# Kernel tuning notes

Hardware: AMD Instinct MI355X
Metric: run time of the kernel (lower is better)

Reference implementation:

```python
import jax, jax.numpy as jnp
import numpy as np

NEG_INF = -1e30  # stands in for torch's -inf diagonal mask; exp() underflows to 0 identically


def conv1x1(x, w, b):
    # x: [B,C,H,W], w: [O,C], b: [O]
    return jnp.einsum('oc,bchw->bohw', w, x) + b[None, :, None, None]


def s_module(x, qw, qb, kw, kb, vw, vb, gamma):
    # CCNet criss-cross attention with -inf diagonal masking on the H branch.
    B, C, H, W = x.shape
    q = conv1x1(x, qw, qb)  # [B,C8,H,W]
    k = conv1x1(x, kw, kb)  # [B,C8,H,W]
    v = conv1x1(x, vw, vb)  # [B,C,H,W]
    # energy_H[b,h,w,g] = <q[b,:,h,w], k[b,:,g,w]>  (attend along column)
    e_h = jnp.einsum('bchw,bcgw->bhwg', q, k)
    diag_mask = jnp.where(jnp.eye(H, dtype=bool), NEG_INF, 0.0).astype(x.dtype)
    e_h = e_h + diag_mask[None, :, None, :]  # mask h == g
    # energy_W[b,h,w,v] = <q[b,:,h,w], k[b,:,h,v]>  (attend along row)
    e_w = jnp.einsum('bchw,bchv->bhwv', q, k)
    att = jax.nn.softmax(jnp.concatenate([e_h, e_w], axis=-1), axis=-1)  # [B,H,W,H+W]
    a_h, a_w = att[..., :H], att[..., H:]
    out_h = jnp.einsum('bcgw,bhwg->bchw', v, a_h)
    out_w = jnp.einsum('bchv,bhwv->bchw', v, a_w)
    return gamma * (out_h + out_w) + x


def cam_module(x, fb, gamma):
    # channel attention: energy [B,C,C], max-sub trick, softmax, bmm back
    B, C, H, W = x.shape
    f = fb.reshape(B, C, H * W)
    energy = jnp.einsum('bcn,bdn->bcd', f, f)
    energy_new = jnp.max(energy, axis=-1, keepdims=True) - energy
    att = jax.nn.softmax(energy_new, axis=-1)
    out = jnp.einsum('bcd,bdn->bcn', att, f).reshape(B, C, H, W)
    return x + gamma * out


def _forward(x, fb, w_conv, b_conv, bn_g, bn_b,
             xq_w, xq_b, xk_w, xk_b, xv_w, xv_b, x_gamma,
             fq_w, fq_b, fk_w, fk_b, fv_w, fv_b, f_gamma,
             pam_gamma, pam_gamma2, cam_gamma):
    # MaxPool2d(kernel=2, stride=2)
    fbd = jax.lax.reduce_window(fb, -jnp.inf, jax.lax.max,
                                (1, 1, 2, 2), (1, 1, 2, 2), 'VALID')
    # convblock: 1x1 conv + BatchNorm (training-mode batch stats) + ReLU
    y = conv1x1(fbd, w_conv, b_conv)
    mu = jnp.mean(y, axis=(0, 2, 3), keepdims=True)
    var = jnp.var(y, axis=(0, 2, 3), keepdims=True)
    y = (y - mu) * jax.lax.rsqrt(var + 1e-5)
    y = y * bn_g[None, :, None, None] + bn_b[None, :, None, None]
    y = jax.nn.relu(y)
    # FeedbackSpatialAttention (PAM)
    x_att = pam_gamma * s_module(x, xq_w, xq_b, xk_w, xk_b, xv_w, xv_b, x_gamma)
    fb_att = s_module(y, fq_w, fq_b, fk_w, fk_b, fv_w, fv_b, f_gamma)
    pam_out = x + x_att + pam_gamma2 * fb_att
    # CAM on (x, processed fb)
    cam_out = cam_module(x, y, cam_gamma)
    return pam_out + cam_out


def setup_inputs() -> dict:
    key = jax.random.key(0)
    ks = jax.random.split(key, 24)
    B, C, H, W = 4, 64, 128, 128
    C8 = C // 8
    d = {
        'x': jax.random.normal(ks[0], (B, C, H, W), jnp.float32),
        'fb': jax.random.normal(ks[1], (B, C, 2 * H, 2 * W), jnp.float32),
        'w_conv': jax.random.normal(ks[2], (C, C), jnp.float32) * 0.05,
        'b_conv': jax.random.normal(ks[3], (C,), jnp.float32) * 0.02,
        'bn_g': jax.random.uniform(ks[4], (C,), jnp.float32, 0.5, 1.5),
        'bn_b': jax.random.normal(ks[5], (C,), jnp.float32) * 0.02,
        'xq_w': jax.random.normal(ks[6], (C8, C), jnp.float32) * 0.05,
        'xq_b': jax.random.normal(ks[7], (C8,), jnp.float32) * 0.02,
        'xk_w': jax.random.normal(ks[8], (C8, C), jnp.float32) * 0.05,
        'xk_b': jax.random.normal(ks[9], (C8,), jnp.float32) * 0.02,
        'xv_w': jax.random.normal(ks[10], (C, C), jnp.float32) * 0.05,
        'xv_b': jax.random.normal(ks[11], (C,), jnp.float32) * 0.02,
        'x_gamma': jax.random.normal(ks[12], (1,), jnp.float32) * 0.1,
        'fq_w': jax.random.normal(ks[13], (C8, C), jnp.float32) * 0.05,
        'fq_b': jax.random.normal(ks[14], (C8,), jnp.float32) * 0.02,
        'fk_w': jax.random.normal(ks[15], (C8, C), jnp.float32) * 0.05,
        'fk_b': jax.random.normal(ks[16], (C8,), jnp.float32) * 0.02,
        'fv_w': jax.random.normal(ks[17], (C, C), jnp.float32) * 0.05,
        'fv_b': jax.random.normal(ks[18], (C,), jnp.float32) * 0.02,
        'f_gamma': jax.random.normal(ks[19], (1,), jnp.float32) * 0.1,
        'pam_gamma': jax.random.normal(ks[20], (1,), jnp.float32) * 0.1,
        'pam_gamma2': jax.random.normal(ks[21], (1,), jnp.float32) * 0.1,
        'cam_gamma': jax.random.normal(ks[22], (1,), jnp.float32) * 0.1,
    }
    return d


def reference(x, fb, w_conv, b_conv, bn_g, bn_b,
              xq_w, xq_b, xk_w, xk_b, xv_w, xv_b, x_gamma,
              fq_w, fq_b, fk_w, fk_b, fv_w, fv_b, f_gamma,
              pam_gamma, pam_gamma2, cam_gamma):
    return _forward(x, fb, w_conv, b_conv, bn_g, bn_b,
                    xq_w, xq_b, xk_w, xk_b, xv_w, xv_b, x_gamma,
                    fq_w, fq_b, fk_w, fk_b, fv_w, fv_b, f_gamma,
                    pam_gamma, pam_gamma2, cam_gamma)
```

## Files before the change

### kernel.cpp

```cpp
#include <hip/hip_runtime.h>
#include <hip/hip_bf16.h>

#define NP 16384
#define NB 4

typedef __hip_bfloat16 bf16;
typedef unsigned short u16;
typedef unsigned short us8 __attribute__((ext_vector_type(8)));
typedef unsigned short us4 __attribute__((ext_vector_type(4)));
typedef short ss8 __attribute__((ext_vector_type(8)));
typedef float f32x4 __attribute__((ext_vector_type(4)));
__device__ __forceinline__ float bf2f(const bf16 v) { return __bfloat162float(v); }
__device__ __forceinline__ bf16 f2bf(float v) { return __float2bfloat16(v); }
__device__ __forceinline__ float bfu(u16 h) {
  return __uint_as_float(((unsigned)h) << 16);
}
__device__ __forceinline__ u16 fbu(float v) {
  bf16 b = f2bf(v);
  return *(u16*)&b;
}


__global__ __launch_bounds__(256, 4) void k_pool_conv(
    const float* __restrict__ fb, const float* __restrict__ wconv,
    const float* __restrict__ bconv, bf16* __restrict__ Y) {
  __shared__ __align__(16) u16 Xs[64 * 64];
  __shared__ __align__(16) u16 wHi[64 * 64], wLo[64 * 64];
  __shared__ float bS[64];
  int tid = threadIdx.x;
  int b = blockIdx.x >> 8, tile = blockIdx.x & 255;
  int n0 = tile * 64;
  int h = n0 >> 7, w0 = n0 & 127;
  for (int i = tid; i < 4096; i += 256) {
    int oc = i >> 6, c = i & 63;
    float wv = wconv[oc * 64 + c];
    u16 hb = fbu(wv);
    u16 lb = fbu(wv - bfu(hb));
    int idx = i ^ ((oc & 7) << 3);
    wHi[idx] = hb;
    wLo[idx] = lb;
  }
  if (tid < 64) bS[tid] = bconv[tid];
  for (int i2 = tid; i2 < 2048; i2 += 256) {
    int c = i2 >> 5, pp = i2 & 31;
    const float* r0 =
        fb + ((size_t)((b * 64 + c) * 256 + 2 * h)) * 256 + 2 * w0 + 4 * pp;
    float4 v0 = *(const float4*)r0;
    float4 v1 = *(const float4*)(r0 + 256);
    int px = 2 * pp;
    float a0 = fmaxf(fmaxf(v0.x, v0.y), fmaxf(v1.x, v1.y));
    float a1 = fmaxf(fmaxf(v0.z, v0.w), fmaxf(v1.z, v1.w));
    Xs[(px * 64 + c) ^ ((((px & 7) ^ ((px >> 3) & 7))) << 3)] = fbu(a0);
    px++;
    Xs[(px * 64 + c) ^ ((((px & 7) ^ ((px >> 3) & 7))) << 3)] = fbu(a1);
  }
  __syncthreads();
  int lane = tid & 63, wv = tid >> 6;
  int il = lane & 15, gq = lane >> 4;
  int pxb = wv * 16;
  ss8 afr[2];
#pragma unroll
  for (int ks = 0; ks < 2; ++ks) {
    int px = pxb + il;
    int idx =
        (px * 64 + ks * 32 + gq * 8) ^ ((((px & 7) ^ ((px >> 3) & 7))) << 3);
    afr[ks] = *(const ss8*)&Xs[idx];
  }
#pragma unroll
  for (int oct = 0; oct < 4; ++oct) {
    int oc = oct * 16 + il;
    ss8 wh[2], wl[2];
#pragma unroll
    for (int ks = 0; ks < 2; ++ks) {
      int idx = (oc * 64 + ks * 32 + gq * 8) ^ ((oc & 7) << 3);
      wh[ks] = *(const ss8*)&wHi[idx];
      wl[ks] = *(const ss8*)&wLo[idx];
    }
    float bv = bS[oc];
    f32x4 acc = {bv, bv, bv, bv};
#pragma unroll
    for (int ks = 0; ks < 2; ++ks) {
      acc = __builtin_amdgcn_mfma_f32_16x16x32_bf16(afr[ks], wh[ks], acc, 0, 0, 0);
      acc = __builtin_amdgcn_mfma_f32_16x16x32_bf16(afr[ks], wl[ks], acc, 0, 0, 0);
    }
    int px0 = pxb + gq * 4;
    us4 ov;
#pragma unroll
    for (int r = 0; r < 4; ++r) ov[r] = fbu(acc[r]);
    *(us4*)(Y + (size_t)(b * 64 + oc) * NP + n0 + px0) = ov;
  }
}

__global__ __launch_bounds__(256) void k_stats_p1(const bf16* __restrict__ Y,
                                                  float* __restrict__ PS) {
  int blk = blockIdx.x, tid = threadIdx.x;
  int o = blk >> 3, slab = blk & 7;
  int b = slab >> 1, half = slab & 1;
  const us8* vp =
      (const us8*)(Y + ((size_t)(b * 64 + o)) * NP + half * 8192);
  float s = 0.f, ss = 0.f;
#pragma unroll
  for (int it = 0; it < 4; ++it) {
    us8 v = vp[tid + 256 * it];
#pragma unroll
    for (int e = 0; e < 8; ++e) {
      float f = bfu(v[e]);
      s += f;
      ss = fmaf(f, f, ss);
    }
  }
  for (int off = 32; off > 0; off >>= 1) {
    s += __shfl_down(s, off, 64);
    ss += __shfl_down(ss, off, 64);
  }
  __shared__ float sh[8];
  int wv = tid >> 6, ln = tid & 63;
  if (ln == 0) { sh[wv] = s; sh[4 + wv] = ss; }
  __syncthreads();
  if (tid == 0) {
    PS[blk] = sh[0] + sh[1] + sh[2] + sh[3];
    PS[512 + blk] = sh[4] + sh[5] + sh[6] + sh[7];
  }
}

__global__ __launch_bounds__(64) void k_stats_p2(
    const float* __restrict__ PS, const float* __restrict__ bng,
    const float* __restrict__ bnb, float* __restrict__ SCALE,
    float* __restrict__ SHIFT, const float* xg, const float* fg,
    const float* pg, const float* pg2, const float* cg,
    float* __restrict__ HDR) {
  int o = threadIdx.x;
  float s = 0.f, ss = 0.f;
#pragma unroll
  for (int k = 0; k < 8; ++k) {
    s += PS[o * 8 + k];
    ss += PS[512 + o * 8 + k];
  }
  const float inv = 1.0f / (NB * NP);
  float mu = s * inv;
  float var = ss * inv - mu * mu;
  float r = rsqrtf(var + 1e-5f);
  float sc = r * bng[o];
  SCALE[o] = sc;
  SHIFT[o] = bnb[o] - mu * sc;
  if (o == 0) {
    float vpg = pg[0];
    HDR[1] = vpg * xg[0];
    HDR[2] = pg2[0] * fg[0];
    HDR[3] = 2.0f + vpg;
    HDR[4] = pg2[0];
    HDR[5] = cg[0];
  }
}

__global__ __launch_bounds__(256, 4) void k_conv_mfma(
    const float* __restrict__ xin, const bf16* __restrict__ Yin,
    const float* __restrict__ SCALE, const float* __restrict__ SHIFT,
    const float* __restrict__ qw0, const float* __restrict__ qb0,
    const float* __restrict__ kw0, const float* __restrict__ kb0,
    const float* __restrict__ vw0, const float* __restrict__ vb0,
    const float* __restrict__ qw1, const float* __restrict__ qb1,
    const float* __restrict__ kw1, const float* __restrict__ kb1,
    const float* __restrict__ vw1, const float* __restrict__ vb1,
    bf16* __restrict__ QK, bf16* __restrict__ V) {
  __shared__ __align__(16) u16 Xs[128 * 64];
  __shared__ __align__(16) u16 wHi[80 * 64], wLo[80 * 64];
  __shared__ float bS[80];
  int tid = threadIdx.x;
  int m = blockIdx.x >> 9;
  int b = (blockIdx.x >> 7) & 3;
  int tile = blockIdx.x & 127;
  int n0 = tile * 128;
  const float* qw = m ? qw1 : qw0;
  const float* qb = m ? qb1 : qb0;
  const float* kw = m ? kw1 : kw0;
  const float* kb = m ? kb1 : kb0;
  const float* vw = m ? vw1 : vw0;
  const float* vb = m ? vb1 : vb0;
  for (int i = tid; i < 5120; i += 256) {
    int oc = i >> 6, c = i & 63;
    float w;
    if (oc < 8) w = qw[oc * 64 + c];
    else if (oc < 16) w = kw[(oc - 8) * 64 + c];
    else w = vw[(oc - 16) * 64 + c];
    u16 hb = fbu(w);
    u16 lb = fbu(w - bfu(hb));
    int idx = (oc * 64 + c) ^ ((oc & 7) << 3);
    wHi[idx] = hb;
    wLo[idx] = lb;
  }
  if (tid < 80)
    bS[tid] = (tid < 8) ? qb[tid] : (tid < 16) ? kb[tid - 8] : vb[tid - 16];
  if (m) {
    for (int i2 = tid; i2 < 1024; i2 += 256) {
      int c = i2 >> 4, vj = i2 & 15;
      us8 v = *(const us8*)(Yin + (size_t)(b * 64 + c) * NP + n0 + vj * 8);
      float sc = SCALE[c], sh = SHIFT[c];
#pragma unroll
      for (int e = 0; e < 8; ++e) {
        int px = vj * 8 + e;
        float f = fmaxf(fmaf(bfu(v[e]), sc, sh), 0.f);
        Xs[(px * 64 + c) ^ ((((px & 7) ^ ((px >> 3) & 7))) << 3)] = fbu(f);
      }
    }
  } else {
    for (int i2 = tid; i2 < 2048; i2 += 256) {
      int c = i2 >> 5, vj = i2 & 31;
      float4 v = *(const float4*)(xin + (size_t)(b * 64 + c) * NP + n0 + vj * 4);
      float vv[4] = {v.x, v.y, v.z, v.w};
#pragma unroll
      for (int r = 0; r < 4; ++r) {
        int px = vj * 4 + r;
        Xs[(px * 64 + c) ^ ((((px & 7) ^ ((px >> 3) & 7))) << 3)] = fbu(vv[r]);
      }
    }
  }
  __syncthreads();
  int lane = tid & 63, wv = tid >> 6;
  int il = lane & 15, gq = lane >> 4;
  int pxb = wv * 32;
  ss8 afr[2][2];
#pragma unroll
  for (int sub = 0; sub < 2; ++sub)
#pragma unroll
    for (int ks = 0; ks < 2; ++ks) {
      int px = pxb + sub * 16 + il;
      int idx =
          (px * 64 + ks * 32 + gq * 8) ^ ((((px & 7) ^ ((px >> 3) & 7))) << 3);
      afr[sub][ks] = *(const ss8*)&Xs[idx];
    }
#pragma unroll
  for (int oct = 0; oct < 5; ++oct) {
    int oc = oct * 16 + il;
    ss8 wh[2], wl[2];
#pragma unroll
    for (int ks = 0; ks < 2; ++ks) {
      int idx = (oc * 64 + ks * 32 + gq * 8) ^ ((oc & 7) << 3);
      wh[ks] = *(const ss8*)&wHi[idx];
      wl[ks] = *(const ss8*)&wLo[idx];
    }
    float bv = bS[oc];
    bf16* dst;
    size_t basep;
    if (oc < 8) { dst = QK; basep = (size_t)(((m * 2 + 0) * 4 + b) * 8 + oc) * NP; }
    else if (oc < 16) { dst = QK; basep = (size_t)(((m * 2 + 1) * 4 + b) * 8 + (oc - 8)) * NP; }
    else { dst = V; basep = (size_t)((m * 4 + b) * 64 + (oc - 16)) * NP; }
#pragma unroll
    for (int sub = 0; sub < 2; ++sub) {
      f32x4 acc = {bv, bv, bv, bv};
#pragma unroll
      for (int ks = 0; ks < 2; ++ks) {
        acc = __builtin_amdgcn_mfma_f32_16x16x32_bf16(afr[sub][ks], wh[ks], acc, 0, 0, 0);
        acc = __builtin_amdgcn_mfma_f32_16x16x32_bf16(afr[sub][ks], wl[ks], acc, 0, 0, 0);
      }
      int px0 = pxb + sub * 16 + gq * 4;
      us4 ov;
#pragma unroll
      for (int r = 0; r < 4; ++r) ov[r] = fbu(acc[r]);
      *(us4*)(dst + basep + n0 + px0) = ov;
    }
  }
}

__global__ __launch_bounds__(256) void k_transpose2(
    const u16* __restrict__ inA, u16* __restrict__ outA,
    const u16* __restrict__ inB, u16* __restrict__ outB, int nA) {
  int tileId = blockIdx.x & 15;
  int plane = blockIdx.x >> 4;
  const u16* ip;
  u16* op;
  if (plane < nA) {
    ip = inA + (size_t)plane * NP;
    op = outA + (size_t)plane * NP;
  } else {
    ip = inB + (size_t)(plane - nA) * NP;
    op = outB + (size_t)(plane - nA) * NP;
  }
  int th = tileId >> 2, tw = tileId & 3;
  __shared__ u16 t[32][33];
  int lx = threadIdx.x & 31, ly = threadIdx.x >> 5;
  for (int i = 0; i < 32; i += 8)
    t[ly + i][lx] = ip[(size_t)(th * 32 + ly + i) * 128 + tw * 32 + lx];
  __syncthreads();
  for (int i = 0; i < 32; i += 8)
    op[(size_t)(tw * 32 + ly + i) * 128 + th * 32 + lx] = t[lx][ly + i];
}

__global__ __launch_bounds__(256, 4) void k_av(
    const bf16* __restrict__ QK, const bf16* __restrict__ QKT,
    const bf16* __restrict__ V, const bf16* __restrict__ VT,
    float* __restrict__ MWp, float* __restrict__ LWp,
    float* __restrict__ MHp, float* __restrict__ LHp,
    float* __restrict__ OW, bf16* __restrict__ OHT) {
  int blk = blockIdx.x;
  int m = blk & 1, mode = (blk >> 1) & 1;
  int bid = blk >> 2;
  int b = bid >> 7, h = bid & 127;
  const bf16* qkbase = mode ? QKT : QK;
  const bf16* Qp = qkbase + (size_t)(((m * 2 + 0) * 4 + b) * 8) * NP;
  const bf16* Kp = qkbase + (size_t)(((m * 2 + 1) * 4 + b) * 8) * NP;
  const bf16* Vp = (mode ? VT : V) + (size_t)((m * 4 + b) * 64) * NP;
  __shared__ __align__(16) u16 qT[128 * 8];
  __shared__ __align__(16) u16 kT[128 * 8];
  __shared__ __align__(16) u16 Vs[64 * 136];
  int tid = threadIdx.x;
  {
    int c = (tid >> 4) & 7, vj = tid & 15;
    const bf16* src = (tid < 128) ? Qp : Kp;
    u16* dst = (tid < 128) ? qT : kT;
    const us8* sp = (const us8*)(src + (size_t)c * NP + (size_t)h * 128);
    us8 sv = sp[vj];
#pragma unroll
    for (int e = 0; e < 8; ++e) {
      int j = vj * 8 + e;
      int p = ((j & 7) << 4) | (j >> 3);
      dst[p * 8 + c] = sv[e];
    }
  }
  for (int i2 = tid; i2 < 1024; i2 += 256) {
    int c = i2 >> 4, vj = i2 & 15;
    const us8* vp = (const us8*)(Vp + (size_t)c * NP + (size_t)h * 128);
    us8 vv = vp[vj];
    *(us8*)&Vs[c * 136 + vj * 8] = vv;
  }
  __syncthreads();
  int lane = tid & 63, wv = tid >> 6;
  int il = lane & 15, gq = lane >> 4;
  size_t sb = (size_t)(m * 4 + b) * NP;
  float* owBase = OW + (size_t)((m * 4 + b) * 64) * NP + (size_t)h * 128;
  bf16* ohBase = OHT + (size_t)((m * 4 + b) * 64) * NP + (size_t)h * 128;
#pragma unroll
  for (int sub = 0; sub < 2; ++sub) {
    int ib = wv * 32 + sub * 16;
    int i = ib + il;
    int pi = ((i & 7) << 4) | (i >> 3);
    us8 qv = *(const us8*)&qT[pi * 8];
    float qr[8];
#pragma unroll
    for (int c = 0; c < 8; ++c) qr[c] = bfu(qv[c]);
    float scr[4][8];
    float mrow = -3.0e38f;
#pragma unroll
    for (int ks = 0; ks < 4; ++ks) {
#pragma unroll
      for (int e = 0; e < 8; ++e) {
        int j = ks * 32 + gq * 8 + e;
        int pj = ((j & 7) << 4) | (j >> 3);
        us8 kv = *(const us8*)&kT[pj * 8];
        float s = 0.f;
#pragma unroll
        for (int c = 0; c < 8; ++c) s = fmaf(qr[c], bfu(kv[c]), s);
        if (mode && j == i) s = -1.0e30f;
        scr[ks][e] = s;
        mrow = fmaxf(mrow, s);
      }
    }
    mrow = fmaxf(mrow, __shfl_xor(mrow, 16, 64));
    mrow = fmaxf(mrow, __shfl_xor(mrow, 32, 64));
    float l = 0.f;
    ss8 afr[4];
#pragma unroll
    for (int ks = 0; ks < 4; ++ks) {
      ss8 af;
#pragma unroll
      for (int e = 0; e < 8; ++e) {
        float ev = __expf(scr[ks][e] - mrow);
        l += ev;
        af[e] = (short)fbu(ev);
      }
      afr[ks] = af;
    }
    l += __shfl_xor(l, 16, 64);
    l += __shfl_xor(l, 32, 64);
    if (gq == 0) {
      if (mode == 0) {
        MWp[sb + (size_t)h * 128 + i] = mrow;
        LWp[sb + (size_t)h * 128 + i] = l;
      } else {
        MHp[sb + (size_t)i * 128 + h] = mrow;
        LHp[sb + (size_t)i * 128 + h] = l;
      }
    }
#pragma unroll
    for (int ct = 0; ct < 4; ++ct) {
      f32x4 acc = {0.f, 0.f, 0.f, 0.f};
#pragma unroll
      for (int ks = 0; ks < 4; ++ks) {
        ss8 bv = *(const ss8*)&Vs[(ct * 16 + il) * 136 + ks * 32 + gq * 8];
        acc = __builtin_amdgcn_mfma_f32_16x16x32_bf16(afr[ks], bv, acc, 0, 0, 0);
      }
      int cch = ct * 16 + il;
      int i0 = ib + gq * 4;
      if (mode == 0) {
#pragma unroll
        for (int r = 0; r < 4; ++r)
          owBase[(size_t)cch * NP + (size_t)(i0 + r)] = acc[r];
      } else {
#pragma unroll
        for (int r = 0; r < 4; ++r)
          ohBase[(size_t)cch * NP + (size_t)(i0 + r)] = f2bf(acc[r]);
      }
    }
  }
}

__global__ __launch_bounds__(256) void k_merge2(
    const bf16* __restrict__ OHT, const float* __restrict__ OW,
    const float* __restrict__ MWp, const float* __restrict__ LWp,
    const float* __restrict__ MHp, const float* __restrict__ LHp,
    const float* __restrict__ HDR, float* __restrict__ ACC) {
  int tileId = blockIdx.x & 15;
  int plane = blockIdx.x >> 4;
  int b = plane >> 6;
  int th = tileId >> 2, tw = tileId & 3;
  __shared__ float t0[32][33], t1[32][33];
  int lx = threadIdx.x & 31, ly = threadIdx.x >> 5;
  const bf16* ip0 = OHT + (size_t)plane * NP;
  const bf16* ip1 = OHT + (size_t)(256 + plane) * NP;
  for (int i = 0; i < 32; i += 8) {
    size_t idx = (size_t)(th * 32 + ly + i) * 128 + tw * 32 + lx;
    t0[ly + i][lx] = bf2f(ip0[idx]);
    t1[ly + i][lx] = bf2f(ip1[idx]);
  }
  __syncthreads();
  float sc0 = HDR[1], sc1 = HDR[2];
  float* op = ACC + (size_t)plane * NP;
  const float* ow0 = OW + (size_t)plane * NP;
  const float* ow1 = OW + (size_t)(256 + plane) * NP;
  size_t s0 = (size_t)b * NP, s1 = (size_t)(4 + b) * NP;
  for (int i = 0; i < 32; i += 8) {
    int hh = tw * 32 + ly + i, ww = th * 32 + lx;
    size_t idx = (size_t)hh * 128 + ww;
    float mw0 = MWp[s0 + idx], mh0 = MHp[s0 + idx];
    float M0 = fmaxf(mw0, mh0);
    float ea0 = __expf(mw0 - M0), eb0 = __expf(mh0 - M0);
    float inv0 = 1.0f / (LWp[s0 + idx] * ea0 + LHp[s0 + idx] * eb0);
    float v0 = (ea0 * ow0[idx] + eb0 * t0[lx][ly + i]) * inv0;
    float mw1 = MWp[s1 + idx], mh1 = MHp[s1 + idx];
    float M1 = fmaxf(mw1, mh1);
    float ea1 = __expf(mw1 - M1), eb1 = __expf(mh1 - M1);
    float inv1 = 1.0f / (LWp[s1 + idx] * ea1 + LHp[s1 + idx] * eb1);
    float v1 = (ea1 * ow1[idx] + eb1 * t1[lx][ly + i]) * inv1;
    op[idx] = sc0 * v0 + sc1 * v1;
  }
}

__global__ __launch_bounds__(256) void k_gram(const bf16* __restrict__ Y,
                                              const float* __restrict__ SCALE,
                                              const float* __restrict__ SHIFT,
                                              float* __restrict__ GP) {
  int b = blockIdx.x >> 7, ch = (blockIdx.x >> 2) & 31, t = blockIdx.x & 3;
  int tid = threadIdx.x;
  __shared__ float fs[64 * 129];
  int cg = tid >> 4, dg = tid & 15;
  float acc[4][4];
#pragma unroll
  for (int i = 0; i < 4; ++i)
#pragma unroll
    for (int jx = 0; jx < 4; ++jx) acc[i][jx] = 0.f;
  const bf16* yb = Y + (size_t)b * 64 * NP + ch * 512;
  for (int idx = tid; idx < 8192; idx += 256) {
    int c = idx >> 7, j = idx & 127;
    float v = fmaf(bf2f(yb[(size_t)c * NP + t * 128 + j]), SCALE[c], SHIFT[c]);
    fs[c * 129 + j] = fmaxf(v, 0.f);
  }
  __syncthreads();
  for (int j = 0; j < 128; ++j) {
    float a[4], d[4];
#pragma unroll
    for (int i = 0; i < 4; ++i) a[i] = fs[(cg * 4 + i) * 129 + j];
#pragma unroll
    for (int i = 0; i < 4; ++i) d[i] = fs[(dg * 4 + i) * 129 + j];
#pragma unroll
    for (int i = 0; i < 4; ++i)
#pragma unroll
      for (int jx = 0; jx < 4; ++jx) acc[i][jx] = fmaf(a[i], d[jx], acc[i][jx]);
  }
  float* gp = GP + ((size_t)(b * 128) + ch * 4 + t) * 4096;
#pragma unroll
  for (int i = 0; i < 4; ++i)
#pragma unroll
    for (int jx = 0; jx < 4; ++jx)
      gp[(cg * 4 + i) * 64 + dg * 4 + jx] = acc[i][jx];
}

__global__ __launch_bounds__(256) void k_gram_reduce(const float* __restrict__ GP,
                                                     float* __restrict__ CATT) {
  int b = blockIdx.x >> 4, rg = blockIdx.x & 15;
  int tid = threadIdx.x;
  __shared__ float Es[256];
  int e = rg * 256 + tid;
  float s = 0.f;
  for (int k = 0; k < 128; ++k) s += GP[((size_t)b * 128 + k) * 4096 + e];
  Es[tid] = s;
  __syncthreads();
  int wv = tid >> 6, ln = tid & 63;
  float v = Es[wv * 64 + ln];
  float mn = v;
  for (int off = 32; off; off >>= 1) mn = fminf(mn, __shfl_xor(mn, off, 64));
  float ev = __expf(mn - v);
  float ssum = ev;
  for (int off = 32; off; off >>= 1) ssum += __shfl_xor(ssum, off, 64);
  CATT[((size_t)b * 64 + rg * 4 + wv) * 64 + ln] = ev / ssum;
}

__global__ __launch_bounds__(256) void k_final(
    const float* __restrict__ x, const bf16* __restrict__ Y,
    const float* __restrict__ SCALE, const float* __restrict__ SHIFT,
    const float* __restrict__ CATT, const float* __restrict__ HDR,
    float* __restrict__ OUT) {
  __shared__ float attS[64 * 65], Ys[64 * 65];
  int tid = threadIdx.x;
  int b = blockIdx.x >> 8, tile = blockIdx.x & 255;
  int n0 = tile * 64;
  for (int i = tid; i < 4096; i += 256)
    attS[(i >> 6) * 65 + (i & 63)] = CATT[(size_t)b * 4096 + i];
  for (int i = tid; i < 4096; i += 256) {
    int d = i >> 6, px = i & 63;
    float v = fmaf(bf2f(Y[(size_t)(b * 64 + d) * NP + n0 + px]), SCALE[d], SHIFT[d]);
    Ys[d * 65 + px] = fmaxf(v, 0.f);
  }
  __syncthreads();
  int cg = tid >> 4, pgx = tid & 15;
  int c0 = cg * 4, p0 = pgx * 4;
  float acc[4][4];
#pragma unroll
  for (int i = 0; i < 4; ++i)
#pragma unroll
    for (int j = 0; j < 4; ++j) acc[i][j] = 0.f;
  for (int d = 0; d < 64; ++d) {
    float a[4], yv[4];
#pragma unroll
    for (int i = 0; i < 4; ++i) a[i] = attS[(c0 + i) * 65 + d];
#pragma unroll
    for (int j = 0; j < 4; ++j) yv[j] = Ys[d * 65 + p0 + j];
#pragma unroll
    for (int i = 0; i < 4; ++i)
#pragma unroll
      for (int j = 0; j < 4; ++j) acc[i][j] = fmaf(a[i], yv[j], acc[i][j]);
  }
  float c2pg = HDR[3], fpg2 = HDR[4], fcg = HDR[5];
#pragma unroll
  for (int i = 0; i < 4; ++i) {
    size_t base = (size_t)(b * 64 + c0 + i) * NP + n0 + p0;
#pragma unroll
    for (int j = 0; j < 4; ++j) {
      float yv = Ys[(c0 + i) * 65 + p0 + j];
      OUT[base + j] =
          c2pg * x[base + j] + fpg2 * yv + OUT[base + j] + fcg * acc[i][j];
    }
  }
}

extern "C" void kernel_launch(void* const* d_in, const int* in_sizes, int n_in,
                              void* d_out, int out_size, void* d_ws, size_t ws_size,
                              hipStream_t stream) {
  const float* x = (const float*)d_in[0];
  const float* fbp = (const float*)d_in[1];

  char* base = (char*)d_ws;
  float* HDR = (float*)base;
  float* SCALE = HDR + 16;
  float* SHIFT = SCALE + 64;
  char* p = base + 4096;
  bf16* Y = (bf16*)p;    p += 8388608;
  bf16* QK = (bf16*)p;   p += 4194304;
  bf16* QKT = (bf16*)p;  p += 4194304;
  bf16* V = (bf16*)p;    p += 16777216;
  bf16* VT = (bf16*)p;   p += 16777216;
  float* MWp = (float*)p; p += 524288;
  float* LWp = (float*)p; p += 524288;
  float* MHp = (float*)p; p += 524288;
  float* LHp = (float*)p; p += 524288;
  bf16* OHT = (bf16*)p;  p += 16777216;
  float* OW = (float*)p; p += 33554432;
  float* GP = (float*)p; p += 8388608;
  float* CATT = (float*)p; p += 1048576;
  float* ACC = (float*)d_out;
  float* PS = (float*)QK;

  k_pool_conv<<<1024, 256, 0, stream>>>(fbp, (const float*)d_in[2],
                                        (const float*)d_in[3], Y);
  k_stats_p1<<<512, 256, 0, stream>>>(Y, PS);
  k_stats_p2<<<1, 64, 0, stream>>>(PS, (const float*)d_in[4],
                                   (const float*)d_in[5], SCALE, SHIFT,
                                   (const float*)d_in[12], (const float*)d_in[19],
                                   (const float*)d_in[20], (const float*)d_in[21],
                                   (const float*)d_in[22], HDR);

  k_conv_mfma<<<1024, 256, 0, stream>>>(
      x, Y, SCALE, SHIFT,
      (const float*)d_in[6], (const float*)d_in[7], (const float*)d_in[8],
      (const float*)d_in[9], (const float*)d_in[10], (const float*)d_in[11],
      (const float*)d_in[13], (const float*)d_in[14], (const float*)d_in[15],
      (const float*)d_in[16], (const float*)d_in[17], (const float*)d_in[18],
      QK, V);
  k_transpose2<<<10240, 256, 0, stream>>>((const u16*)QK, (u16*)QKT,
                                          (const u16*)V, (u16*)VT, 128);
  k_av<<<2048, 256, 0, stream>>>(QK, QKT, V, VT, MWp, LWp, MHp, LHp, OW, OHT);
  k_merge2<<<4096, 256, 0, stream>>>(OHT, OW, MWp, LWp, MHp, LHp, HDR, ACC);

  k_gram<<<512, 256, 0, stream>>>(Y, SCALE, SHIFT, GP);
  k_gram_reduce<<<64, 256, 0, stream>>>(GP, CATT);
  k_final<<<1024, 256, 0, stream>>>(x, Y, SCALE, SHIFT, CATT, HDR,
                                    (float*)d_out);
}
```

Measured before the change: 277.4 us.

## Fuse BN stats into pool-conv, merge gram into conv, store OW as bf16

The BatchNorm partial sums now come straight from the MFMA accumulators inside the pool+conv kernel, so the separate pass that re-reads Y for statistics is gone. The second stats kernel reduces 1024 per-block partials. The gram kernel is merged into the QKV conv launch as extra blocks, and the gram reduction is merged into the merge kernel, which cuts the launch count. The W-branch output is stored in bf16 instead of fp32, halving that round-trip's traffic at some cost in precision.

Result: slower. 384.0 us (+38.4%).

```diff
diff --git a/kernel.cpp b/kernel.cpp
--- a/kernel.cpp
+++ b/kernel.cpp
@@ -23,17 +23,19 @@
 
 __global__ __launch_bounds__(256, 4) void k_pool_conv(
     const float* __restrict__ fb, const float* __restrict__ wconv,
-    const float* __restrict__ bconv, bf16* __restrict__ Y) {
+    const float* __restrict__ bconv, bf16* __restrict__ Y,
+    float* __restrict__ PS) {
   __shared__ __align__(16) u16 Xs[64 * 64];
   __shared__ __align__(16) u16 wHi[64 * 64], wLo[64 * 64];
   __shared__ float bS[64];
+  __shared__ float redS[256], redSS[256];
   int tid = threadIdx.x;
   int b = blockIdx.x >> 8, tile = blockIdx.x & 255;
   int n0 = tile * 64;
   int h = n0 >> 7, w0 = n0 & 127;
   for (int i = tid; i < 4096; i += 256) {
-    int oc = i >> 6, c = i & 63;
-    float wv = wconv[oc * 64 + c];
+    int oc = i >> 6;
+    float wv = wconv[i];
     u16 hb = fbu(wv);
     u16 lb = fbu(wv - bfu(hb));
     int idx = i ^ ((oc & 7) << 3);
@@ -55,9 +57,9 @@
     Xs[(px * 64 + c) ^ ((((px & 7) ^ ((px >> 3) & 7))) << 3)] = fbu(a1);
   }
   __syncthreads();
-  int lane = tid & 63, wv = tid >> 6;
+  int lane = tid & 63, wvid = tid >> 6;
   int il = lane & 15, gq = lane >> 4;
-  int pxb = wv * 16;
+  int pxb = wvid * 16;
   ss8 afr[2];
 #pragma unroll
   for (int ks = 0; ks < 2; ++ks) {
@@ -88,72 +90,61 @@
 #pragma unroll
     for (int r = 0; r < 4; ++r) ov[r] = fbu(acc[r]);
     *(us4*)(Y + (size_t)(b * 64 + oc) * NP + n0 + px0) = ov;
-  }
-}
-
-__global__ __launch_bounds__(256) void k_stats_p1(const bf16* __restrict__ Y,
-                                                  float* __restrict__ PS) {
-  int blk = blockIdx.x, tid = threadIdx.x;
-  int o = blk >> 3, slab = blk & 7;
-  int b = slab >> 1, half = slab & 1;
-  const us8* vp =
-      (const us8*)(Y + ((size_t)(b * 64 + o)) * NP + half * 8192);
-  float s = 0.f, ss = 0.f;
-#pragma unroll
-  for (int it = 0; it < 4; ++it) {
-    us8 v = vp[tid + 256 * it];
-#pragma unroll
-    for (int e = 0; e < 8; ++e) {
-      float f = bfu(v[e]);
-      s += f;
-      ss = fmaf(f, f, ss);
-    }
-  }
-  for (int off = 32; off > 0; off >>= 1) {
-    s += __shfl_down(s, off, 64);
-    ss += __shfl_down(ss, off, 64);
-  }
-  __shared__ float sh[8];
-  int wv = tid >> 6, ln = tid & 63;
-  if (ln == 0) { sh[wv] = s; sh[4 + wv] = ss; }
-  __syncthreads();
-  if (tid == 0) {
-    PS[blk] = sh[0] + sh[1] + sh[2] + sh[3];
-    PS[512 + blk] = sh[4] + sh[5] + sh[6] + sh[7];
-  }
-}
-
-__global__ __launch_bounds__(64) void k_stats_p2(
+    float s_oc = (acc[0] + acc[1]) + (acc[2] + acc[3]);
+    float ss_oc = fmaf(acc[0], acc[0],
+                  fmaf(acc[1], acc[1], fmaf(acc[2], acc[2], acc[3] * acc[3])));
+    s_oc += __shfl_xor(s_oc, 16, 64);
+    s_oc += __shfl_xor(s_oc, 32, 64);
+    ss_oc += __shfl_xor(ss_oc, 16, 64);
+    ss_oc += __shfl_xor(ss_oc, 32, 64);
+    if (gq == 0) { redS[wvid * 64 + oc] = s_oc; redSS[wvid * 64 + oc] = ss_oc; }
+  }
+  __syncthreads();
+  if (tid < 128) {
+    int st = tid >> 6, oc = tid & 63;
+    const float* rr = st ? redSS : redS;
+    PS[(size_t)blockIdx.x * 128 + tid] =
+        (rr[oc] + rr[64 + oc]) + (rr[128 + oc] + rr[192 + oc]);
+  }
+}
+
+__global__ __launch_bounds__(256) void k_stats_p2(
     const float* __restrict__ PS, const float* __restrict__ bng,
     const float* __restrict__ bnb, float* __restrict__ SCALE,
     float* __restrict__ SHIFT, const float* xg, const float* fg,
     const float* pg, const float* pg2, const float* cg,
     float* __restrict__ HDR) {
-  int o = threadIdx.x;
-  float s = 0.f, ss = 0.f;
-#pragma unroll
-  for (int k = 0; k < 8; ++k) {
-    s += PS[o * 8 + k];
-    ss += PS[512 + o * 8 + k];
-  }
-  const float inv = 1.0f / (NB * NP);
-  float mu = s * inv;
-  float var = ss * inv - mu * mu;
-  float r = rsqrtf(var + 1e-5f);
-  float sc = r * bng[o];
-  SCALE[o] = sc;
-  SHIFT[o] = bnb[o] - mu * sc;
-  if (o == 0) {
-    float vpg = pg[0];
-    HDR[1] = vpg * xg[0];
-    HDR[2] = pg2[0] * fg[0];
-    HDR[3] = 2.0f + vpg;
-    HDR[4] = pg2[0];
-    HDR[5] = cg[0];
-  }
-}
-
-__global__ __launch_bounds__(256, 4) void k_conv_mfma(
+  int t = threadIdx.x;
+  __shared__ float sh[256];
+  int s = t & 127, half = t >> 7;
+  float a = 0.f;
+  for (int blk = half * 512; blk < half * 512 + 512; ++blk)
+    a += PS[(size_t)blk * 128 + s];
+  sh[t] = a;
+  __syncthreads();
+  if (t < 128) sh[t] = sh[t] + sh[128 + t];
+  __syncthreads();
+  if (t < 64) {
+    float ssum = sh[t], sqs = sh[64 + t];
+    const float inv = 1.0f / (NB * NP);
+    float mu = ssum * inv;
+    float var = sqs * inv - mu * mu;
+    float r = rsqrtf(var + 1e-5f);
+    float sc = r * bng[t];
+    SCALE[t] = sc;
+    SHIFT[t] = bnb[t] - mu * sc;
+    if (t == 0) {
+      float vpg = pg[0];
+      HDR[1] = vpg * xg[0];
+      HDR[2] = pg2[0] * fg[0];
+      HDR[3] = 2.0f + vpg;
+      HDR[4] = pg2[0];
+      HDR[5] = cg[0];
+    }
+  }
+}
+
+__global__ __launch_bounds__(256, 4) void k_conv_gram(
     const float* __restrict__ xin, const bf16* __restrict__ Yin,
     const float* __restrict__ SCALE, const float* __restrict__ SHIFT,
     const float* __restrict__ qw0, const float* __restrict__ qb0,
@@ -162,103 +153,141 @@
     const float* __restrict__ qw1, const float* __restrict__ qb1,
     const float* __restrict__ kw1, const float* __restrict__ kb1,
     const float* __restrict__ vw1, const float* __restrict__ vb1,
-    bf16* __restrict__ QK, bf16* __restrict__ V) {
-  __shared__ __align__(16) u16 Xs[128 * 64];
-  __shared__ __align__(16) u16 wHi[80 * 64], wLo[80 * 64];
-  __shared__ float bS[80];
+    bf16* __restrict__ QK, bf16* __restrict__ V, float* __restrict__ GP) {
+  __shared__ __align__(16) char SMEM[37248];
   int tid = threadIdx.x;
-  int m = blockIdx.x >> 9;
-  int b = (blockIdx.x >> 7) & 3;
-  int tile = blockIdx.x & 127;
-  int n0 = tile * 128;
-  const float* qw = m ? qw1 : qw0;
-  const float* qb = m ? qb1 : qb0;
-  const float* kw = m ? kw1 : kw0;
-  const float* kb = m ? kb1 : kb0;
-  const float* vw = m ? vw1 : vw0;
-  const float* vb = m ? vb1 : vb0;
-  for (int i = tid; i < 5120; i += 256) {
-    int oc = i >> 6, c = i & 63;
-    float w;
-    if (oc < 8) w = qw[oc * 64 + c];
-    else if (oc < 16) w = kw[(oc - 8) * 64 + c];
-    else w = vw[(oc - 16) * 64 + c];
-    u16 hb = fbu(w);
-    u16 lb = fbu(w - bfu(hb));
-    int idx = (oc * 64 + c) ^ ((oc & 7) << 3);
-    wHi[idx] = hb;
-    wLo[idx] = lb;
-  }
-  if (tid < 80)
-    bS[tid] = (tid < 8) ? qb[tid] : (tid < 16) ? kb[tid - 8] : vb[tid - 16];
-  if (m) {
-    for (int i2 = tid; i2 < 1024; i2 += 256) {
-      int c = i2 >> 4, vj = i2 & 15;
-      us8 v = *(const us8*)(Yin + (size_t)(b * 64 + c) * NP + n0 + vj * 8);
-      float sc = SCALE[c], sh = SHIFT[c];
-#pragma unroll
-      for (int e = 0; e < 8; ++e) {
-        int px = vj * 8 + e;
-        float f = fmaxf(fmaf(bfu(v[e]), sc, sh), 0.f);
-        Xs[(px * 64 + c) ^ ((((px & 7) ^ ((px >> 3) & 7))) << 3)] = fbu(f);
+  if (blockIdx.x < 1024) {
+    u16* Xs = (u16*)SMEM;
+    u16* wHi = (u16*)(SMEM + 16384);
+    u16* wLo = (u16*)(SMEM + 26624);
+    float* bS = (float*)(SMEM + 36864);
+    int m = blockIdx.x >> 9;
+    int b = (blockIdx.x >> 7) & 3;
+    int tile = blockIdx.x & 127;
+    int n0 = tile * 128;
+    const float* qw = m ? qw1 : qw0;
+    const float* qb = m ? qb1 : qb0;
+    const float* kw = m ? kw1 : kw0;
+    const float* kb = m ? kb1 : kb0;
+    const float* vw = m ? vw1 : vw0;
+    const float* vb = m ? vb1 : vb0;
+    for (int i = tid; i < 5120; i += 256) {
+      int oc = i >> 6, c = i & 63;
+      float w;
+      if (oc < 8) w = qw[oc * 64 + c];
+      else if (oc < 16) w = kw[(oc - 8) * 64 + c];
+      else w = vw[(oc - 16) * 64 + c];
+      u16 hb = fbu(w);
+      u16 lb = fbu(w - bfu(hb));
+      int idx = (oc * 64 + c) ^ ((oc & 7) << 3);
+      wHi[idx] = hb;
+      wLo[idx] = lb;
+    }
+    if (tid < 80)
+      bS[tid] = (tid < 8) ? qb[tid] : (tid < 16) ? kb[tid - 8] : vb[tid - 16];
+    if (m) {
+      for (int i2 = tid; i2 < 1024; i2 += 256) {
+        int c = i2 >> 4, vj = i2 & 15;
+        us8 v = *(const us8*)(Yin + (size_t)(b * 64 + c) * NP + n0 + vj * 8);
+        float sc = SCALE[c], sh = SHIFT[c];
+#pragma unroll
+        for (int e = 0; e < 8; ++e) {
+          int px = vj * 8 + e;
+          float f = fmaxf(fmaf(bfu(v[e]), sc, sh), 0.f);
+          Xs[(px * 64 + c) ^ ((((px & 7) ^ ((px >> 3) & 7))) << 3)] = fbu(f);
+        }
+      }
+    } else {
+      for (int i2 = tid; i2 < 2048; i2 += 256) {
+        int c = i2 >> 5, vj = i2 & 31;
+        float4 v = *(const float4*)(xin + (size_t)(b * 64 + c) * NP + n0 + vj * 4);
+        float vv[4] = {v.x, v.y, v.z, v.w};
+#pragma unroll
+        for (int r = 0; r < 4; ++r) {
+          int px = vj * 4 + r;
+          Xs[(px * 64 + c) ^ ((((px & 7) ^ ((px >> 3) & 7))) << 3)] = fbu(vv[r]);
+        }
+      }
+    }
+    __syncthreads();
+    int lane = tid & 63, wvid = tid >> 6;
+    int il = lane & 15, gq = lane >> 4;
+    int pxb = wvid * 32;
+    ss8 afr[2][2];
+#pragma unroll
+    for (int sub = 0; sub < 2; ++sub)
+#pragma unroll
+      for (int ks = 0; ks < 2; ++ks) {
+        int px = pxb + sub * 16 + il;
+        int idx =
+            (px * 64 + ks * 32 + gq * 8) ^ ((((px & 7) ^ ((px >> 3) & 7))) << 3);
+        afr[sub][ks] = *(const ss8*)&Xs[idx];
+      }
+#pragma unroll
+    for (int oct = 0; oct < 5; ++oct) {
+      int oc = oct * 16 + il;
+      ss8 wh[2], wl[2];
+#pragma unroll
+      for (int ks = 0; ks < 2; ++ks) {
+        int idx = (oc * 64 + ks * 32 + gq * 8) ^ ((oc & 7) << 3);
+        wh[ks] = *(const ss8*)&wHi[idx];
+        wl[ks] = *(const ss8*)&wLo[idx];
+      }
+      float bv = bS[oc];
+      bf16* dst;
+      size_t basep;
+      if (oc < 8) { dst = QK; basep = (size_t)(((m * 2 + 0) * 4 + b) * 8 + oc) * NP; }
+      else if (oc < 16) { dst = QK; basep = (size_t)(((m * 2 + 1) * 4 + b) * 8 + (oc - 8)) * NP; }
+      else { dst = V; basep = (size_t)((m * 4 + b) * 64 + (oc - 16)) * NP; }
+#pragma unroll
+      for (int sub = 0; sub < 2; ++sub) {
+        f32x4 acc = {bv, bv, bv, bv};
+#pragma unroll
+        for (int ks = 0; ks < 2; ++ks) {
+          acc = __builtin_amdgcn_mfma_f32_16x16x32_bf16(afr[sub][ks], wh[ks], acc, 0, 0, 0);
+          acc = __builtin_amdgcn_mfma_f32_16x16x32_bf16(afr[sub][ks], wl[ks], acc, 0, 0, 0);
+        }
+        int px0 = pxb + sub * 16 + gq * 4;
+        us4 ov;
+#pragma unroll
+        for (int r = 0; r < 4; ++r) ov[r] = fbu(acc[r]);
+        *(us4*)(dst + basep + n0 + px0) = ov;
       }
     }
   } else {
-    for (int i2 = tid; i2 < 2048; i2 += 256) {
-      int c = i2 >> 5, vj = i2 & 31;
-      float4 v = *(const float4*)(xin + (size_t)(b * 64 + c) * NP + n0 + vj * 4);
-      float vv[4] = {v.x, v.y, v.z, v.w};
-#pragma unroll
-      for (int r = 0; r < 4; ++r) {
-        int px = vj * 4 + r;
-        Xs[(px * 64 + c) ^ ((((px & 7) ^ ((px >> 3) & 7))) << 3)] = fbu(vv[r]);
-      }
-    }
-  }
-  __syncthreads();
-  int lane = tid & 63, wv = tid >> 6;
-  int il = lane & 15, gq = lane >> 4;
-  int pxb = wv * 32;
-  ss8 afr[2][2];
-#pragma unroll
-  for (int sub = 0; sub < 2; ++sub)
-#pragma unroll
-    for (int ks = 0; ks < 2; ++ks) {
-      int px = pxb + sub * 16 + il;
-      int idx =
-          (px * 64 + ks * 32 + gq * 8) ^ ((((px & 7) ^ ((px >> 3) & 7))) << 3);
-      afr[sub][ks] = *(const ss8*)&Xs[idx];
-    }
-#pragma unroll
-  for (int oct = 0; oct < 5; ++oct) {
-    int oc = oct * 16 + il;
-    ss8 wh[2], wl[2];
-#pragma unroll
-    for (int ks = 0; ks < 2; ++ks) {
-      int idx = (oc * 64 + ks * 32 + gq * 8) ^ ((oc & 7) << 3);
-      wh[ks] = *(const ss8*)&wHi[idx];
-      wl[ks] = *(const ss8*)&wLo[idx];
-    }
-    float bv = bS[oc];
-    bf16* dst;
-    size_t basep;
-    if (oc < 8) { dst = QK; basep = (size_t)(((m * 2 + 0) * 4 + b) * 8 + oc) * NP; }
-    else if (oc < 16) { dst = QK; basep = (size_t)(((m * 2 + 1) * 4 + b) * 8 + (oc - 8)) * NP; }
-    else { dst = V; basep = (size_t)((m * 4 + b) * 64 + (oc - 16)) * NP; }
-#pragma unroll
-    for (int sub = 0; sub < 2; ++sub) {
-      f32x4 acc = {bv, bv, bv, bv};
-#pragma unroll
-      for (int ks = 0; ks < 2; ++ks) {
-        acc = __builtin_amdgcn_mfma_f32_16x16x32_bf16(afr[sub][ks], wh[ks], acc, 0, 0, 0);
-        acc = __builtin_amdgcn_mfma_f32_16x16x32_bf16(afr[sub][ks], wl[ks], acc, 0, 0, 0);
-      }
-      int px0 = pxb + sub * 16 + gq * 4;
-      us4 ov;
-#pragma unroll
-      for (int r = 0; r < 4; ++r) ov[r] = fbu(acc[r]);
-      *(us4*)(dst + basep + n0 + px0) = ov;
-    }
+    float* fs = (float*)SMEM;
+    int bid = blockIdx.x - 1024;
+    int b = bid >> 7, ch = (bid >> 2) & 31, t = bid & 3;
+    int cg = tid >> 4, dg = tid & 15;
+    float acc[4][4];
+#pragma unroll
+    for (int i = 0; i < 4; ++i)
+#pragma unroll
+      for (int jx = 0; jx < 4; ++jx) acc[i][jx] = 0.f;
+    const bf16* yb = Yin + (size_t)b * 64 * NP + ch * 512;
+    for (int idx = tid; idx < 8192; idx += 256) {
+      int c = idx >> 7, j = idx & 127;
+      float v = fmaf(bf2f(yb[(size_t)c * NP + t * 128 + j]), SCALE[c], SHIFT[c]);
+      fs[c * 129 + j] = fmaxf(v, 0.f);
+    }
+    __syncthreads();
+    for (int j = 0; j < 128; ++j) {
+      float a[4], d[4];
+#pragma unroll
+      for (int i = 0; i < 4; ++i) a[i] = fs[(cg * 4 + i) * 129 + j];
+#pragma unroll
+      for (int i = 0; i < 4; ++i) d[i] = fs[(dg * 4 + i) * 129 + j];
+#pragma unroll
+      for (int i = 0; i < 4; ++i)
+#pragma unroll
+        for (int jx = 0; jx < 4; ++jx) acc[i][jx] = fmaf(a[i], d[jx], acc[i][jx]);
+    }
+    float* gp = GP + ((size_t)(b * 128) + ch * 4 + t) * 4096;
+#pragma unroll
+    for (int i = 0; i < 4; ++i)
+#pragma unroll
+      for (int jx = 0; jx < 4; ++jx)
+        gp[(cg * 4 + i) * 64 + dg * 4 + jx] = acc[i][jx];
   }
 }
 
@@ -291,7 +320,7 @@
     const bf16* __restrict__ V, const bf16* __restrict__ VT,
     float* __restrict__ MWp, float* __restrict__ LWp,
     float* __restrict__ MHp, float* __restrict__ LHp,
-    float* __restrict__ OW, bf16* __restrict__ OHT) {
+    bf16* __restrict__ OWb, bf16* __restrict__ OHT) {
   int blk = blockIdx.x;
   int m = blk & 1, mode = (blk >> 1) & 1;
   int bid = blk >> 2;
@@ -324,14 +353,14 @@
     *(us8*)&Vs[c * 136 + vj * 8] = vv;
   }
   __syncthreads();
-  int lane = tid & 63, wv = tid >> 6;
+  int lane = tid & 63, wvid = tid >> 6;
   int il = lane & 15, gq = lane >> 4;
   size_t sb = (size_t)(m * 4 + b) * NP;
-  float* owBase = OW + (size_t)((m * 4 + b) * 64) * NP + (size_t)h * 128;
-  bf16* ohBase = OHT + (size_t)((m * 4 + b) * 64) * NP + (size_t)h * 128;
+  bf16* oBase = (mode ? OHT : OWb) + (size_t)((m * 4 + b) * 64) * NP +
+                (size_t)h * 128;
 #pragma unroll
   for (int sub = 0; sub < 2; ++sub) {
-    int ib = wv * 32 + sub * 16;
+    int ib = wvid * 32 + sub * 16;
     int i = ib + il;
     int pi = ((i & 7) << 4) | (i >> 3);
     us8 qv = *(const us8*)&qT[pi * 8];
@@ -391,117 +420,74 @@
       }
       int cch = ct * 16 + il;
       int i0 = ib + gq * 4;
-      if (mode == 0) {
-#pragma unroll
-        for (int r = 0; r < 4; ++r)
-          owBase[(size_t)cch * NP + (size_t)(i0 + r)] = acc[r];
-      } else {
-#pragma unroll
-        for (int r = 0; r < 4; ++r)
-          ohBase[(size_t)cch * NP + (size_t)(i0 + r)] = f2bf(acc[r]);
-      }
-    }
-  }
-}
-
-__global__ __launch_bounds__(256) void k_merge2(
-    const bf16* __restrict__ OHT, const float* __restrict__ OW,
+      us4 ov;
+#pragma unroll
+      for (int r = 0; r < 4; ++r) ov[r] = fbu(acc[r]);
+      *(us4*)(oBase + (size_t)cch * NP + i0) = ov;
+    }
+  }
+}
+
+__global__ __launch_bounds__(256) void k_merge_reduce(
+    const bf16* __restrict__ OHT, const bf16* __restrict__ OWb,
     const float* __restrict__ MWp, const float* __restrict__ LWp,
     const float* __restrict__ MHp, const float* __restrict__ LHp,
-    const float* __restrict__ HDR, float* __restrict__ ACC) {
-  int tileId = blockIdx.x & 15;
-  int plane = blockIdx.x >> 4;
-  int b = plane >> 6;
-  int th = tileId >> 2, tw = tileId & 3;
-  __shared__ float t0[32][33], t1[32][33];
-  int lx = threadIdx.x & 31, ly = threadIdx.x >> 5;
-  const bf16* ip0 = OHT + (size_t)plane * NP;
-  const bf16* ip1 = OHT + (size_t)(256 + plane) * NP;
-  for (int i = 0; i < 32; i += 8) {
-    size_t idx = (size_t)(th * 32 + ly + i) * 128 + tw * 32 + lx;
-    t0[ly + i][lx] = bf2f(ip0[idx]);
-    t1[ly + i][lx] = bf2f(ip1[idx]);
-  }
-  __syncthreads();
-  float sc0 = HDR[1], sc1 = HDR[2];
-  float* op = ACC + (size_t)plane * NP;
-  const float* ow0 = OW + (size_t)plane * NP;
-  const float* ow1 = OW + (size_t)(256 + plane) * NP;
-  size_t s0 = (size_t)b * NP, s1 = (size_t)(4 + b) * NP;
-  for (int i = 0; i < 32; i += 8) {
-    int hh = tw * 32 + ly + i, ww = th * 32 + lx;
-    size_t idx = (size_t)hh * 128 + ww;
-    float mw0 = MWp[s0 + idx], mh0 = MHp[s0 + idx];
-    float M0 = fmaxf(mw0, mh0);
-    float ea0 = __expf(mw0 - M0), eb0 = __expf(mh0 - M0);
-    float inv0 = 1.0f / (LWp[s0 + idx] * ea0 + LHp[s0 + idx] * eb0);
-    float v0 = (ea0 * ow0[idx] + eb0 * t0[lx][ly + i]) * inv0;
-    float mw1 = MWp[s1 + idx], mh1 = MHp[s1 + idx];
-    float M1 = fmaxf(mw1, mh1);
-    float ea1 = __expf(mw1 - M1), eb1 = __expf(mh1 - M1);
-    float inv1 = 1.0f / (LWp[s1 + idx] * ea1 + LHp[s1 + idx] * eb1);
-    float v1 = (ea1 * ow1[idx] + eb1 * t1[lx][ly + i]) * inv1;
-    op[idx] = sc0 * v0 + sc1 * v1;
-  }
-}
-
-__global__ __launch_bounds__(256) void k_gram(const bf16* __restrict__ Y,
-                                              const float* __restrict__ SCALE,
-                                              const float* __restrict__ SHIFT,
-                                              float* __restrict__ GP) {
-  int b = blockIdx.x >> 7, ch = (blockIdx.x >> 2) & 31, t = blockIdx.x & 3;
+    const float* __restrict__ HDR, float* __restrict__ ACC,
+    const float* __restrict__ GP, float* __restrict__ CATT) {
   int tid = threadIdx.x;
-  __shared__ float fs[64 * 129];
-  int cg = tid >> 4, dg = tid & 15;
-  float acc[4][4];
-#pragma unroll
-  for (int i = 0; i < 4; ++i)
-#pragma unroll
-    for (int jx = 0; jx < 4; ++jx) acc[i][jx] = 0.f;
-  const bf16* yb = Y + (size_t)b * 64 * NP + ch * 512;
-  for (int idx = tid; idx < 8192; idx += 256) {
-    int c = idx >> 7, j = idx & 127;
-    float v = fmaf(bf2f(yb[(size_t)c * NP + t * 128 + j]), SCALE[c], SHIFT[c]);
-    fs[c * 129 + j] = fmaxf(v, 0.f);
-  }
-  __syncthreads();
-  for (int j = 0; j < 128; ++j) {
-    float a[4], d[4];
-#pragma unroll
-    for (int i = 0; i < 4; ++i) a[i] = fs[(cg * 4 + i) * 129 + j];
-#pragma unroll
-    for (int i = 0; i < 4; ++i) d[i] = fs[(dg * 4 + i) * 129 + j];
-#pragma unroll
-    for (int i = 0; i < 4; ++i)
-#pragma unroll
-      for (int jx = 0; jx < 4; ++jx) acc[i][jx] = fmaf(a[i], d[jx], acc[i][jx]);
-  }
-  float* gp = GP + ((size_t)(b * 128) + ch * 4 + t) * 4096;
-#pragma unroll
-  for (int i = 0; i < 4; ++i)
-#pragma unroll
-    for (int jx = 0; jx < 4; ++jx)
-      gp[(cg * 4 + i) * 64 + dg * 4 + jx] = acc[i][jx];
-}
-
-__global__ __launch_bounds__(256) void k_gram_reduce(const float* __restrict__ GP,
-                                                     float* __restrict__ CATT) {
-  int b = blockIdx.x >> 4, rg = blockIdx.x & 15;
-  int tid = threadIdx.x;
-  __shared__ float Es[256];
-  int e = rg * 256 + tid;
-  float s = 0.f;
-  for (int k = 0; k < 128; ++k) s += GP[((size_t)b * 128 + k) * 4096 + e];
-  Es[tid] = s;
-  __syncthreads();
-  int wv = tid >> 6, ln = tid & 63;
-  float v = Es[wv * 64 + ln];
-  float mn = v;
-  for (int off = 32; off; off >>= 1) mn = fminf(mn, __shfl_xor(mn, off, 64));
-  float ev = __expf(mn - v);
-  float ssum = ev;
-  for (int off = 32; off; off >>= 1) ssum += __shfl_xor(ssum, off, 64);
-  CATT[((size_t)b * 64 + rg * 4 + wv) * 64 + ln] = ev / ssum;
+  if (blockIdx.x < 4096) {
+    int tileId = blockIdx.x & 15;
+    int plane = blockIdx.x >> 4;
+    int b = plane >> 6;
+    int th = tileId >> 2, tw = tileId & 3;
+    __shared__ float t0[32][33], t1[32][33];
+    int lx = tid & 31, ly = tid >> 5;
+    const bf16* ip0 = OHT + (size_t)plane * NP;
+    const bf16* ip1 = OHT + (size_t)(256 + plane) * NP;
+    for (int i = 0; i < 32; i += 8) {
+      size_t idx = (size_t)(th * 32 + ly + i) * 128 + tw * 32 + lx;
+      t0[ly + i][lx] = bf2f(ip0[idx]);
+      t1[ly + i][lx] = bf2f(ip1[idx]);
+    }
+    __syncthreads();
+    float sc0 = HDR[1], sc1 = HDR[2];
+    float* op = ACC + (size_t)plane * NP;
+    const bf16* ow0 = OWb + (size_t)plane * NP;
+    const bf16* ow1 = OWb + (size_t)(256 + plane) * NP;
+    size_t s0 = (size_t)b * NP, s1 = (size_t)(4 + b) * NP;
+    for (int i = 0; i < 32; i += 8) {
+      int hh = tw * 32 + ly + i, ww = th * 32 + lx;
+      size_t idx = (size_t)hh * 128 + ww;
+      float mw0 = MWp[s0 + idx], mh0 = MHp[s0 + idx];
+      float M0 = fmaxf(mw0, mh0);
+      float ea0 = __expf(mw0 - M0), eb0 = __expf(mh0 - M0);
+      float inv0 = 1.0f / (LWp[s0 + idx] * ea0 + LHp[s0 + idx] * eb0);
+      float v0 = (ea0 * bf2f(ow0[idx]) + eb0 * t0[lx][ly + i]) * inv0;
+      float mw1 = MWp[s1 + idx], mh1 = MHp[s1 + idx];
+      float M1 = fmaxf(mw1, mh1);
+      float ea1 = __expf(mw1 - M1), eb1 = __expf(mh1 - M1);
+      float inv1 = 1.0f / (LWp[s1 + idx] * ea1 + LHp[s1 + idx] * eb1);
+      float v1 = (ea1 * bf2f(ow1[idx]) + eb1 * t1[lx][ly + i]) * inv1;
+      op[idx] = sc0 * v0 + sc1 * v1;
+    }
+  } else {
+    int bid = blockIdx.x - 4096;
+    int b = bid >> 4, rg = bid & 15;
+    __shared__ float Es[256];
+    int e = rg * 256 + tid;
+    float s = 0.f;
+    for (int k = 0; k < 128; ++k) s += GP[((size_t)b * 128 + k) * 4096 + e];
+    Es[tid] = s;
+    __syncthreads();
+    int wvid = tid >> 6, ln = tid & 63;
+    float v = Es[wvid * 64 + ln];
+    float mn = v;
+    for (int off = 32; off; off >>= 1) mn = fminf(mn, __shfl_xor(mn, off, 64));
+    float ev = __expf(mn - v);
+    float ssum = ev;
+    for (int off = 32; off; off >>= 1) ssum += __shfl_xor(ssum, off, 64);
+    CATT[((size_t)b * 64 + rg * 4 + wvid) * 64 + ln] = ev / ssum;
+  }
 }
 
 __global__ __launch_bounds__(256) void k_final(
@@ -573,35 +559,31 @@
   float* MHp = (float*)p; p += 524288;
   float* LHp = (float*)p; p += 524288;
   bf16* OHT = (bf16*)p;  p += 16777216;
-  float* OW = (float*)p; p += 33554432;
+  bf16* OWb = (bf16*)p;  p += 16777216;
   float* GP = (float*)p; p += 8388608;
   float* CATT = (float*)p; p += 1048576;
   float* ACC = (float*)d_out;
   float* PS = (float*)QK;
 
   k_pool_conv<<<1024, 256, 0, stream>>>(fbp, (const float*)d_in[2],
-                                        (const float*)d_in[3], Y);
-  k_stats_p1<<<512, 256, 0, stream>>>(Y, PS);
-  k_stats_p2<<<1, 64, 0, stream>>>(PS, (const float*)d_in[4],
-                                   (const float*)d_in[5], SCALE, SHIFT,
-                                   (const float*)d_in[12], (const float*)d_in[19],
-                                   (const float*)d_in[20], (const float*)d_in[21],
-                                   (const float*)d_in[22], HDR);
-
-  k_conv_mfma<<<1024, 256, 0, stream>>>(
+                                        (const float*)d_in[3], Y, PS);
+  k_stats_p2<<<1, 256, 0, stream>>>(PS, (const float*)d_in[4],
+                                    (const float*)d_in[5], SCALE, SHIFT,
+                                    (const float*)d_in[12], (const float*)d_in[19],
+                                    (const float*)d_in[20], (const float*)d_in[21],
+                                    (const float*)d_in[22], HDR);
+  k_conv_gram<<<1536, 256, 0, stream>>>(
       x, Y, SCALE, SHIFT,
       (const float*)d_in[6], (const float*)d_in[7], (const float*)d_in[8],
       (const float*)d_in[9], (const float*)d_in[10], (const float*)d_in[11],
       (const float*)d_in[13], (const float*)d_in[14], (const float*)d_in[15],
       (const float*)d_in[16], (const float*)d_in[17], (const float*)d_in[18],
-      QK, V);
+      QK, V, GP);
   k_transpose2<<<10240, 256, 0, stream>>>((const u16*)QK, (u16*)QKT,
                                           (const u16*)V, (u16*)VT, 128);
-  k_av<<<2048, 256, 0, stream>>>(QK, QKT, V, VT, MWp, LWp, MHp, LHp, OW, OHT);
-  k_merge2<<<4096, 256, 0, stream>>>(OHT, OW, MWp, LWp, MHp, LHp, HDR, ACC);
-
-  k_gram<<<512, 256, 0, stream>>>(Y, SCALE, SHIFT, GP);
-  k_gram_reduce<<<64, 256, 0, stream>>>(GP, CATT);
+  k_av<<<2048, 256, 0, stream>>>(QK, QKT, V, VT, MWp, LWp, MHp, LHp, OWb, OHT);
+  k_merge_reduce<<<4160, 256, 0, stream>>>(OHT, OWb, MWp, LWp, MHp, LHp, HDR,
+                                           ACC, GP, CATT);
   k_final<<<1024, 256, 0, stream>>>(x, Y, SCALE, SHIFT, CATT, HDR,
                                     (float*)d_out);
 }
```
